# Kernel tuning notes

Measured on AMD Instinct MI355X. Metric: run time of the kernel, lower is better.

Reference implementation:

```python
import jax, jax.numpy as jnp
import numpy as np

B, T, I, H, R, O = 128, 512, 64, 512, 4, 64
NOISE_STD = 0.05
TAU = 0.2


def setup_inputs() -> dict:
    key = jax.random.key(0)
    ks = jax.random.split(key, 16)
    s = 0.08  # xavier-ish scale to keep gates in sane range
    return {
        "u": jax.random.normal(ks[0], (B, T, I), jnp.float32),
        "x0": jnp.zeros((B, H), jnp.float32),
        "noise": jax.random.normal(ks[1], (T, B, H), jnp.float32),
        "W_ir": jax.random.normal(ks[2], (H, I), jnp.float32) * s,
        "b_ir": jax.random.normal(ks[3], (H,), jnp.float32) * s,
        "W_iz": jax.random.normal(ks[4], (H, I), jnp.float32) * s,
        "b_iz": jax.random.normal(ks[5], (H,), jnp.float32) * s,
        "W_ih": jax.random.normal(ks[6], (H, I), jnp.float32) * s,
        "b_ih": jax.random.normal(ks[7], (H,), jnp.float32) * s,
        "N_hr": jax.random.normal(ks[8], (H, R), jnp.float32) * s,
        "M_hr": jax.random.normal(ks[9], (H, R), jnp.float32) * s,
        "N_hz": jax.random.normal(ks[10], (H, R), jnp.float32) * s,
        "M_hz": jax.random.normal(ks[11], (H, R), jnp.float32) * s,
        "N_hh": jax.random.normal(ks[12], (H, R), jnp.float32) * s,
        "M_hh": jax.random.normal(ks[13], (H, R), jnp.float32) * s,
        "W_out": jax.random.normal(ks[14], (O, H), jnp.float32) * s,
        "b_out": jax.random.normal(ks[15], (O,), jnp.float32) * s,
    }


def reference(u, x0, noise, W_ir, b_ir, W_iz, b_iz, W_ih, b_ih,
              N_hr, M_hr, N_hz, M_hz, N_hh, M_hh, W_out, b_out):
    scale = 1.0 / u.shape[-1] * 0 + 1.0 / N_hr.shape[0]  # 1/H (cont mode)
    scale = 1.0 / N_hr.shape[0]
    u_t = jnp.transpose(u, (1, 0, 2))  # [T,B,I]
    # precompute input projections for all steps (same math as per-step Linear)
    ir = jnp.einsum('tbi,hi->tbh', u_t, W_ir) + b_ir
    iz = jnp.einsum('tbi,hi->tbh', u_t, W_iz) + b_iz
    ih = jnp.einsum('tbi,hi->tbh', u_t, W_ih) + b_ih

    def step(x, inp):
        ir_t, iz_t, ih_t, n_t = inp
        hr = (x @ N_hr) @ M_hr.T * scale
        hz = (x @ N_hz) @ M_hz.T * scale
        r = jax.nn.sigmoid(ir_t + hr)
        z = jax.nn.sigmoid(iz_t + hz)
        hh = ((r * x) @ N_hh) @ M_hh.T * scale
        g = jnp.tanh(ih_t + hh)
        rec_x = (1.0 - z) * g + z * x
        x_new = x + NOISE_STD * n_t + TAU * (-x + rec_x)  # cont mode
        return x_new, x_new

    x_last, traj = jax.lax.scan(step, x0, (ir, iz, ih, noise))  # traj: [T,B,H]
    traj = jnp.transpose(traj, (1, 0, 2))  # [B,T,H]
    output = jnp.einsum('bth,oh->bto', traj, W_out) + b_out
    return output, x_last, traj
```

## Files before the change

kernel.cpp:

```cpp
#include <hip/hip_runtime.h>
#include <hip/hip_bf16.h>
#include <stdint.h>

#define Bv 128
#define Tv 512
#define Iv 64
#define Hv 512
#define Ov 64

typedef __attribute__((ext_vector_type(8))) short bv8;
typedef __attribute__((ext_vector_type(4))) float fv4;
typedef __attribute__((ext_vector_type(2))) float fv2;
typedef __attribute__((ext_vector_type(4))) unsigned uv4;
typedef __attribute__((ext_vector_type(2))) unsigned uv2;
typedef __attribute__((ext_vector_type(8))) unsigned short usv8;

#define LOG2E 1.44269504f
#define TWOLOG2E 2.88539008f

static __device__ __forceinline__ unsigned short f2bf(float f) {
  unsigned u = __builtin_bit_cast(unsigned, f);
  u += 0x7fffu + ((u >> 16) & 1u);
  return (unsigned short)(u >> 16);
}
static __device__ __forceinline__ float bf2f(unsigned short s) {
  return __builtin_bit_cast(float, ((unsigned)s) << 16);
}
static __device__ __forceinline__ fv2 pkfma(fv2 a, fv2 b, fv2 c) {
  return __builtin_elementwise_fma(a, b, c);
}

static __device__ __forceinline__ float wave_red(float v) {
  float d;
  asm("v_add_f32_dpp %0, %1, %1 quad_perm:[1,0,3,2] row_mask:0xf bank_mask:0xf"
      : "=v"(d) : "v"(v)); v = d;
  asm("v_add_f32_dpp %0, %1, %1 quad_perm:[2,3,0,1] row_mask:0xf bank_mask:0xf"
      : "=v"(d) : "v"(v)); v = d;
  asm("v_add_f32_dpp %0, %1, %1 row_ror:4 row_mask:0xf bank_mask:0xf"
      : "=v"(d) : "v"(v)); v = d;
  asm("v_add_f32_dpp %0, %1, %1 row_ror:8 row_mask:0xf bank_mask:0xf"
      : "=v"(d) : "v"(v)); v = d;
  unsigned a = __builtin_bit_cast(unsigned, v);
  uv2 p = __builtin_amdgcn_permlane16_swap(a, a, false, false);
  v = __builtin_bit_cast(float, p[0]) + __builtin_bit_cast(float, p[1]);
  a = __builtin_bit_cast(unsigned, v);
  uv2 q = __builtin_amdgcn_permlane32_swap(a, a, false, false);
  v = __builtin_bit_cast(float, q[0]) + __builtin_bit_cast(float, q[1]);
  return v;
}

__global__ __launch_bounds__(256) void proj_kernel(
    const float* __restrict__ u,
    const float* __restrict__ Wir, const float* __restrict__ bir,
    const float* __restrict__ Wiz, const float* __restrict__ biz,
    const float* __restrict__ Wih, const float* __restrict__ bih,
    unsigned* __restrict__ irz, unsigned short* __restrict__ ihb)
{
  __shared__ __align__(16) unsigned short As[64][72];
  const int bt0 = blockIdx.x * 64;
  const int h0b = blockIdx.y * 64;
  const int tid = threadIdx.x;
  {
    const int r = tid >> 2, ksg = (tid & 3) * 16;
    const float* src = u + (size_t)(bt0 + r) * Iv + ksg;
    unsigned short tmp[16];
#pragma unroll
    for (int i = 0; i < 16; i += 4) {
      float4 v = *(const float4*)(src + i);
      tmp[i] = f2bf(v.x); tmp[i+1] = f2bf(v.y); tmp[i+2] = f2bf(v.z); tmp[i+3] = f2bf(v.w);
    }
    *(uv4*)&As[r][ksg]     = *(uv4*)&tmp[0];
    *(uv4*)&As[r][ksg + 8] = *(uv4*)&tmp[8];
  }
  __syncthreads();
  const int wave = tid >> 6, lane = tid & 63;
  const int n = lane & 15, q = lane >> 4;
  const int h = h0b + wave * 16 + n;
  const float* Wg[3] = {Wir, Wiz, Wih};
  const float SCL[3] = {-LOG2E, -LOG2E, -TWOLOG2E};
  bv8 bfrag[3][2];
#pragma unroll
  for (int g = 0; g < 3; ++g)
#pragma unroll
    for (int ks = 0; ks < 2; ++ks) {
      const float* wp = Wg[g] + (size_t)h * Iv + ks * 32 + q * 8;
      float4 w0 = *(const float4*)wp, w1 = *(const float4*)(wp + 4);
      const float s = SCL[g];
      bv8 f;
      f[0] = (short)f2bf(w0.x * s); f[1] = (short)f2bf(w0.y * s);
      f[2] = (short)f2bf(w0.z * s); f[3] = (short)f2bf(w0.w * s);
      f[4] = (short)f2bf(w1.x * s); f[5] = (short)f2bf(w1.y * s);
      f[6] = (short)f2bf(w1.z * s); f[7] = (short)f2bf(w1.w * s);
      bfrag[g][ks] = f;
    }
  const float bs0 = bir[h] * -LOG2E, bs1 = biz[h] * -LOG2E, bs2 = bih[h] * -TWOLOG2E;
#pragma unroll
  for (int sub = 0; sub < 4; ++sub) {
    bv8 a0 = *(const bv8*)&As[sub * 16 + n][q * 8];
    bv8 a1 = *(const bv8*)&As[sub * 16 + n][32 + q * 8];
    fv4 ar = {0.f,0.f,0.f,0.f}, az = {0.f,0.f,0.f,0.f}, ah = {0.f,0.f,0.f,0.f};
    ar = __builtin_amdgcn_mfma_f32_16x16x32_bf16(a0, bfrag[0][0], ar, 0, 0, 0);
    ar = __builtin_amdgcn_mfma_f32_16x16x32_bf16(a1, bfrag[0][1], ar, 0, 0, 0);
    az = __builtin_amdgcn_mfma_f32_16x16x32_bf16(a0, bfrag[1][0], az, 0, 0, 0);
    az = __builtin_amdgcn_mfma_f32_16x16x32_bf16(a1, bfrag[1][1], az, 0, 0, 0);
    ah = __builtin_amdgcn_mfma_f32_16x16x32_bf16(a0, bfrag[2][0], ah, 0, 0, 0);
    ah = __builtin_amdgcn_mfma_f32_16x16x32_bf16(a1, bfrag[2][1], ah, 0, 0, 0);
#pragma unroll
    for (int j = 0; j < 4; ++j) {
      const int row = bt0 + sub * 16 + q * 4 + j;
      const size_t slot = (size_t)row * Hv + h;
      irz[slot] = ((unsigned)f2bf(az[j] + bs1) << 16) | (unsigned)f2bf(ar[j] + bs0);
      ihb[slot] = f2bf(ah[j] + bs2);
    }
  }
}

struct Buf { uv4 irz0, irz1; usv8 ih; fv4 nz0, nz1; };
#define IRZ(bf, j) ((j) < 4 ? (bf).irz0[(j)] : (bf).irz1[(j) - 4])
#define NZE(bf, j) ((j) < 4 ? (bf).nz0[(j)]  : (bf).nz1[(j) - 4])

__global__ __launch_bounds__(64, 1) void scan_kernel(
    const float* __restrict__ x0, const float* __restrict__ noise,
    const float* __restrict__ Nhr, const float* __restrict__ Mhr,
    const float* __restrict__ Nhz, const float* __restrict__ Mhz,
    const float* __restrict__ Nhh, const float* __restrict__ Mhh,
    unsigned* __restrict__ traj, const unsigned short* __restrict__ ihb,
    float* __restrict__ xlast)
{
  __shared__ __align__(16) float S[7 * 2048];
  const int b = blockIdx.x, lane = threadIdx.x;
  const int h0 = lane * 8;
  const int xr = (lane & 7) * 4;

  int fo[8];
#pragma unroll
  for (int j = 0; j < 8; ++j) fo[j] = lane * 32 + ((j * 4) ^ xr);

#define LDQ(sec, j) (*(const fv4*)&S[(sec) * 2048 + fo[j]])

  {
    const float smr = -(1.0f / 512.0f) * LOG2E;
    const float smh = -(1.0f / 512.0f) * TWOLOG2E;
#pragma unroll
    for (int j = 0; j < 8; ++j) {
      *(fv4*)&S[0 * 2048 + fo[j]] = *(const fv4*)(Nhr + (size_t)(h0 + j) * 4);
      *(fv4*)&S[1 * 2048 + fo[j]] = *(const fv4*)(Nhz + (size_t)(h0 + j) * 4);
      *(fv4*)&S[2 * 2048 + fo[j]] = *(const fv4*)(Nhh + (size_t)(h0 + j) * 4);
      fv4 mr = *(const fv4*)(Mhr + (size_t)(h0 + j) * 4) * smr;
      fv4 mz = *(const fv4*)(Mhz + (size_t)(h0 + j) * 4) * smr;
      fv4 q0 = {mr[0], mz[0], mr[1], mz[1]};
      fv4 q1 = {mr[2], mz[2], mr[3], mz[3]};
      *(fv4*)&S[3 * 2048 + fo[j]] = q0;
      *(fv4*)&S[4 * 2048 + fo[j]] = q1;
    }
#pragma unroll
    for (int p = 0; p < 4; ++p) {
      fv4 a = *(const fv4*)(Mhh + (size_t)(h0 + 2 * p) * 4) * smh;
      fv4 c = *(const fv4*)(Mhh + (size_t)(h0 + 2 * p + 1) * 4) * smh;
      fv4 q0 = {a[0], c[0], a[1], c[1]};
      fv4 q1 = {a[2], c[2], a[3], c[3]};
      *(fv4*)&S[5 * 2048 + fo[p]] = q0;
      *(fv4*)&S[6 * 2048 + fo[p]] = q1;
    }
  }

  float x[8];
  {
    const float* xp = x0 + (size_t)b * Hv;
    fv4 a = *(const fv4*)(xp + h0);
    fv4 c = *(const fv4*)(xp + h0 + 4);
#pragma unroll
    for (int j = 0; j < 4; ++j) { x[j] = a[j]; x[j + 4] = c[j]; }
  }
  const unsigned* trajU = traj + (size_t)b * Tv * Hv;
  const unsigned short* ihU = ihb + (size_t)b * Tv * Hv;
  const float* noiseU = noise + (size_t)b * Hv;

  Buf A, Bb;
  auto LOAD = [&](Buf& bf, int t) {
    const unsigned* pr = trajU + (size_t)t * Hv;
    bf.irz0 = *(const uv4*)(pr + h0);
    bf.irz1 = *(const uv4*)(pr + h0 + 4);
    const unsigned short* pi = ihU + (size_t)t * Hv;
    bf.ih = *(const usv8*)(pi + h0);
    const float* pn = noiseU + (size_t)t * (Bv * Hv);
    bf.nz0 = *(const fv4*)(pn + h0);
    bf.nz1 = *(const fv4*)(pn + h0 + 4);
  };
  auto PIN = [&](Buf& bf) {
    asm volatile("" : "+v"(bf.irz0), "+v"(bf.irz1), "+v"(bf.ih),
                      "+v"(bf.nz0), "+v"(bf.nz1));
  };
  auto STEP = [&](const Buf& bf, int t) {
    fv2 sr01 = {0.f,0.f}, sr23 = {0.f,0.f}, sz01 = {0.f,0.f}, sz23 = {0.f,0.f};
#pragma unroll
    for (int j = 0; j < 8; ++j) {
      fv4 nrj = LDQ(0, j), nzj = LDQ(1, j);
      fv2 xs = {x[j], x[j]};
      sr01 = pkfma(xs, fv2{nrj[0], nrj[1]}, sr01);
      sr23 = pkfma(xs, fv2{nrj[2], nrj[3]}, sr23);
      sz01 = pkfma(xs, fv2{nzj[0], nzj[1]}, sz01);
      sz23 = pkfma(xs, fv2{nzj[2], nzj[3]}, sz23);
    }
    float sr[4] = {sr01[0], sr01[1], sr23[0], sr23[1]};
    float sz[4] = {sz01[0], sz01[1], sz23[0], sz23[1]};
#pragma unroll
    for (int r = 0; r < 4; ++r) { sr[r] = wave_red(sr[r]); sz[r] = wave_red(sz[r]); }
    fv2 srz[4];
#pragma unroll
    for (int r = 0; r < 4; ++r) srz[r] = fv2{sr[r], sz[r]};
    float rxv[8], w02[8];
#pragma unroll
    for (int j = 0; j < 8; ++j) {
      fv4 q0 = LDQ(3, j), q1 = LDQ(4, j);
      fv2 h2 = fv2{q1[2], q1[3]} * srz[3];
      h2 = pkfma(fv2{q1[0], q1[1]}, srz[2], h2);
      h2 = pkfma(fv2{q0[2], q0[3]}, srz[1], h2);
      h2 = pkfma(fv2{q0[0], q0[1]}, srz[0], h2);
      unsigned w = IRZ(bf, j);
      float tr = h2[0] + __builtin_bit_cast(float, w << 16);
      float tz = h2[1] + __builtin_bit_cast(float, w & 0xffff0000u);
      float er = __builtin_amdgcn_exp2f(tr);
      float ez = __builtin_amdgcn_exp2f(tz);
      float Ar = 1.0f + er, Az = 1.0f + ez;
      float R = __builtin_amdgcn_rcpf(Ar * Az);
      rxv[j] = (R * Az) * x[j];
      w02[j] = fmaf(R * Ar, -0.2f, 0.2f);
    }
    fv2 sh01 = {0.f,0.f}, sh23 = {0.f,0.f};
#pragma unroll
    for (int j = 0; j < 8; ++j) {
      fv4 nhj = LDQ(2, j);
      fv2 xs = {rxv[j], rxv[j]};
      sh01 = pkfma(xs, fv2{nhj[0], nhj[1]}, sh01);
      sh23 = pkfma(xs, fv2{nhj[2], nhj[3]}, sh23);
    }
    fv2 sh2[4];
    {
      float s0 = wave_red(sh01[0]), s1 = wave_red(sh01[1]);
      float s2 = wave_red(sh23[0]), s3 = wave_red(sh23[1]);
      sh2[0] = fv2{s0, s0}; sh2[1] = fv2{s1, s1};
      sh2[2] = fv2{s2, s2}; sh2[3] = fv2{s3, s3};
    }
#pragma unroll
    for (int p = 0; p < 4; ++p) {
      fv4 q0 = LDQ(5, p), q1 = LDQ(6, p);
      fv2 hh = fv2{q1[2], q1[3]} * sh2[3];
      hh = pkfma(fv2{q1[0], q1[1]}, sh2[2], hh);
      hh = pkfma(fv2{q0[2], q0[3]}, sh2[1], hh);
      hh = pkfma(fv2{q0[0], q0[1]}, sh2[0], hh);
      const int j0 = 2 * p, j1 = 2 * p + 1;
      float t0 = fminf(hh[0] + bf2f(bf.ih[j0]), 44.0f);
      float t1 = fminf(hh[1] + bf2f(bf.ih[j1]), 44.0f);
      float e0 = __builtin_amdgcn_exp2f(t0);
      float e1 = __builtin_amdgcn_exp2f(t1);
      float A0 = 1.0f + e0, A1 = 1.0f + e1;
      float R = __builtin_amdgcn_rcpf(A0 * A1);
      float g0 = (1.0f - e0) * A1 * R;
      float g1 = (1.0f - e1) * A0 * R;
      float d0 = g0 - x[j0], d1 = g1 - x[j1];
      x[j0] = fmaf(0.05f, NZE(bf, j0), x[j0]);
      x[j0] = fmaf(w02[j0], d0, x[j0]);
      x[j1] = fmaf(0.05f, NZE(bf, j1), x[j1]);
      x[j1] = fmaf(w02[j1], d1, x[j1]);
    }
    float* po = (float*)(trajU + (size_t)t * Hv);
    fv4 s0 = {x[0], x[1], x[2], x[3]}, s1 = {x[4], x[5], x[6], x[7]};
    *(fv4*)(po + h0) = s0;
    *(fv4*)(po + h0 + 4) = s1;
  };
  LOAD(A, 0);
  for (int t = 0; t < Tv; t += 2) {
    LOAD(Bb, t + 1);
    STEP(A, t);
    PIN(Bb);
    if (t + 2 < Tv) LOAD(A, t + 2);
    STEP(Bb, t + 1);
    PIN(A);
  }
  {
    float* xp = xlast + (size_t)b * Hv;
    fv4 s0 = {x[0], x[1], x[2], x[3]}, s1 = {x[4], x[5], x[6], x[7]};
    *(fv4*)(xp + h0) = s0;
    *(fv4*)(xp + h0 + 4) = s1;
  }
#undef LDQ
}

__global__ __launch_bounds__(256) void outproj_kernel(
    const float* __restrict__ traj, const float* __restrict__ Wout,
    const float* __restrict__ bout, float* __restrict__ out)
{
  __shared__ __align__(16) unsigned short As[64][40];
  const int bt0 = blockIdx.x * 64;
  const int tid = threadIdx.x;
  const int wave = tid >> 6, lane = tid & 63;
  const int n = lane & 15, q = lane >> 4;
  const int o = wave * 16 + n;
  const float bo = bout[o];
  fv4 acc[4] = {{0.f,0.f,0.f,0.f},{0.f,0.f,0.f,0.f},{0.f,0.f,0.f,0.f},{0.f,0.f,0.f,0.f}};
  const int r = tid >> 2, ksg = (tid & 3) * 8;
  for (int ks = 0; ks < 16; ++ks) {
    __syncthreads();
    {
      const float* src = traj + (size_t)(bt0 + r) * Hv + ks * 32 + ksg;
      float4 v0 = *(const float4*)src, v1 = *(const float4*)(src + 4);
      unsigned short tmp[8];
      tmp[0] = f2bf(v0.x); tmp[1] = f2bf(v0.y); tmp[2] = f2bf(v0.z); tmp[3] = f2bf(v0.w);
      tmp[4] = f2bf(v1.x); tmp[5] = f2bf(v1.y); tmp[6] = f2bf(v1.z); tmp[7] = f2bf(v1.w);
      *(uv4*)&As[r][ksg] = *(uv4*)&tmp[0];
    }
    __syncthreads();
    const float* wp = Wout + (size_t)o * Hv + ks * 32 + q * 8;
    float4 w0 = *(const float4*)wp, w1 = *(const float4*)(wp + 4);
    bv8 bf;
    bf[0] = (short)f2bf(w0.x); bf[1] = (short)f2bf(w0.y);
    bf[2] = (short)f2bf(w0.z); bf[3] = (short)f2bf(w0.w);
    bf[4] = (short)f2bf(w1.x); bf[5] = (short)f2bf(w1.y);
    bf[6] = (short)f2bf(w1.z); bf[7] = (short)f2bf(w1.w);
#pragma unroll
    for (int sub = 0; sub < 4; ++sub) {
      bv8 af = *(const bv8*)&As[sub * 16 + n][q * 8];
      acc[sub] = __builtin_amdgcn_mfma_f32_16x16x32_bf16(af, bf, acc[sub], 0, 0, 0);
    }
  }
#pragma unroll
  for (int sub = 0; sub < 4; ++sub)
#pragma unroll
    for (int j = 0; j < 4; ++j) {
      const int row = bt0 + sub * 16 + q * 4 + j;
      out[(size_t)row * Ov + o] = acc[sub][j] + bo;
    }
}

extern "C" void kernel_launch(void* const* d_in, const int* in_sizes, int n_in,
                              void* d_out, int out_size, void* d_ws, size_t ws_size,
                              hipStream_t stream) {
  const float* u    = (const float*)d_in[0];
  const float* x0   = (const float*)d_in[1];
  const float* noise= (const float*)d_in[2];
  const float* Wir  = (const float*)d_in[3];
  const float* bir  = (const float*)d_in[4];
  const float* Wiz  = (const float*)d_in[5];
  const float* biz  = (const float*)d_in[6];
  const float* Wih  = (const float*)d_in[7];
  const float* bih  = (const float*)d_in[8];
  const float* Nhr  = (const float*)d_in[9];
  const float* Mhr  = (const float*)d_in[10];
  const float* Nhz  = (const float*)d_in[11];
  const float* Mhz  = (const float*)d_in[12];
  const float* Nhh  = (const float*)d_in[13];
  const float* Mhh  = (const float*)d_in[14];
  const float* Wout = (const float*)d_in[15];
  const float* bout = (const float*)d_in[16];

  float* out   = (float*)d_out;
  float* xlast = out + (size_t)Bv * Tv * Ov;
  float* traj  = xlast + (size_t)Bv * Hv;
  unsigned short* ihbuf = (unsigned short*)d_ws;

  proj_kernel<<<dim3(1024, 8, 1), 256, 0, stream>>>(
      u, Wir, bir, Wiz, biz, Wih, bih, (unsigned*)traj, ihbuf);
  scan_kernel<<<dim3(128, 1, 1), 64, 0, stream>>>(
      x0, noise, Nhr, Mhr, Nhz, Mhz, Nhh, Mhh, (unsigned*)traj, ihbuf, xlast);
  outproj_kernel<<<dim3(1024, 1, 1), 256, 0, stream>>>(traj, Wout, bout, out);
}
```

Baseline: 833.8 us.

## Stream per-step scan inputs into LDS via global_load_lds double buffering

The scan kernel's per-step prefetch of gate pre-activations, the ih projection and noise used to go through registers in a two-buffer scheme. It now uses direct global-to-LDS 16-byte DMA loads into two LDS stream buffers, issued two steps ahead. An explicit vmcnt wait gates the reads, and the data is read back from LDS just before use. This is meant to free VGPRs and hide global latency on the serial recurrence, at the cost of extra LDS round trips and a hand-tuned waitcnt count that depends on stores also counting in vmcnt. The Mhh coefficient table is also packed into one LDS section.

```diff
diff --git a/kernel.cpp b/kernel.cpp
--- a/kernel.cpp
+++ b/kernel.cpp
@@ -28,6 +28,12 @@
 }
 static __device__ __forceinline__ fv2 pkfma(fv2 a, fv2 b, fv2 c) {
   return __builtin_elementwise_fma(a, b, c);
+}
+
+static __device__ __forceinline__ void dma16(const void* g, void* l) {
+  __builtin_amdgcn_global_load_lds(
+      (const __attribute__((address_space(1))) void*)g,
+      (__attribute__((address_space(3))) void*)l, 16, 0, 0);
 }
 
 static __device__ __forceinline__ float wave_red(float v) {
@@ -115,9 +121,14 @@
   }
 }
 
-struct Buf { uv4 irz0, irz1; usv8 ih; fv4 nz0, nz1; };
-#define IRZ(bf, j) ((j) < 4 ? (bf).irz0[(j)] : (bf).irz1[(j) - 4])
-#define NZE(bf, j) ((j) < 4 ? (bf).nz0[(j)]  : (bf).nz1[(j) - 4])
+#define OFF_NR 0
+#define OFF_NZ 2048
+#define OFF_NH 4096
+#define OFF_MRZ0 6144
+#define OFF_MRZ1 8192
+#define OFF_MH2 10240
+#define STREAM0 49152
+#define STREAM_SZ 5120
 
 __global__ __launch_bounds__(64, 1) void scan_kernel(
     const float* __restrict__ x0, const float* __restrict__ noise,
@@ -127,31 +138,33 @@
     unsigned* __restrict__ traj, const unsigned short* __restrict__ ihb,
     float* __restrict__ xlast)
 {
-  __shared__ __align__(16) float S[7 * 2048];
+  __shared__ __align__(16) float S[12288 + 2560];
   const int b = blockIdx.x, lane = threadIdx.x;
   const int h0 = lane * 8;
   const int xr = (lane & 7) * 4;
+  const int lofs16 = lane * 16;
+  const int lofs32 = lane * 32;
 
   int fo[8];
 #pragma unroll
   for (int j = 0; j < 8; ++j) fo[j] = lane * 32 + ((j * 4) ^ xr);
 
-#define LDQ(sec, j) (*(const fv4*)&S[(sec) * 2048 + fo[j]])
+#define LDQ(sec, j) (*(const fv4*)&S[(sec) + fo[j]])
 
   {
     const float smr = -(1.0f / 512.0f) * LOG2E;
     const float smh = -(1.0f / 512.0f) * TWOLOG2E;
 #pragma unroll
     for (int j = 0; j < 8; ++j) {
-      *(fv4*)&S[0 * 2048 + fo[j]] = *(const fv4*)(Nhr + (size_t)(h0 + j) * 4);
-      *(fv4*)&S[1 * 2048 + fo[j]] = *(const fv4*)(Nhz + (size_t)(h0 + j) * 4);
-      *(fv4*)&S[2 * 2048 + fo[j]] = *(const fv4*)(Nhh + (size_t)(h0 + j) * 4);
+      *(fv4*)&S[OFF_NR + fo[j]] = *(const fv4*)(Nhr + (size_t)(h0 + j) * 4);
+      *(fv4*)&S[OFF_NZ + fo[j]] = *(const fv4*)(Nhz + (size_t)(h0 + j) * 4);
+      *(fv4*)&S[OFF_NH + fo[j]] = *(const fv4*)(Nhh + (size_t)(h0 + j) * 4);
       fv4 mr = *(const fv4*)(Mhr + (size_t)(h0 + j) * 4) * smr;
       fv4 mz = *(const fv4*)(Mhz + (size_t)(h0 + j) * 4) * smr;
       fv4 q0 = {mr[0], mz[0], mr[1], mz[1]};
       fv4 q1 = {mr[2], mz[2], mr[3], mz[3]};
-      *(fv4*)&S[3 * 2048 + fo[j]] = q0;
-      *(fv4*)&S[4 * 2048 + fo[j]] = q1;
+      *(fv4*)&S[OFF_MRZ0 + fo[j]] = q0;
+      *(fv4*)&S[OFF_MRZ1 + fo[j]] = q1;
     }
 #pragma unroll
     for (int p = 0; p < 4; ++p) {
@@ -159,8 +172,8 @@
       fv4 c = *(const fv4*)(Mhh + (size_t)(h0 + 2 * p + 1) * 4) * smh;
       fv4 q0 = {a[0], c[0], a[1], c[1]};
       fv4 q1 = {a[2], c[2], a[3], c[3]};
-      *(fv4*)&S[5 * 2048 + fo[p]] = q0;
-      *(fv4*)&S[6 * 2048 + fo[p]] = q1;
+      *(fv4*)&S[OFF_MH2 + fo[p]]     = q0;
+      *(fv4*)&S[OFF_MH2 + fo[p + 4]] = q1;
     }
   }
 
@@ -175,27 +188,24 @@
   const unsigned* trajU = traj + (size_t)b * Tv * Hv;
   const unsigned short* ihU = ihb + (size_t)b * Tv * Hv;
   const float* noiseU = noise + (size_t)b * Hv;
-
-  Buf A, Bb;
-  auto LOAD = [&](Buf& bf, int t) {
-    const unsigned* pr = trajU + (size_t)t * Hv;
-    bf.irz0 = *(const uv4*)(pr + h0);
-    bf.irz1 = *(const uv4*)(pr + h0 + 4);
-    const unsigned short* pi = ihU + (size_t)t * Hv;
-    bf.ih = *(const usv8*)(pi + h0);
-    const float* pn = noiseU + (size_t)t * (Bv * Hv);
-    bf.nz0 = *(const fv4*)(pn + h0);
-    bf.nz1 = *(const fv4*)(pn + h0 + 4);
+  char* Sb = (char*)S;
+
+  auto ISSUE = [&](int sb, int t) {
+    const char* g1 = (const char*)(trajU + (size_t)t * Hv) + lofs16;
+    dma16(g1,        Sb + sb);
+    dma16(g1 + 1024, Sb + sb + 1024);
+    const char* g2 = (const char*)(ihU + (size_t)t * Hv) + lofs16;
+    dma16(g2,        Sb + sb + 2048);
+    const char* g3 = (const char*)(noiseU + (size_t)t * (Bv * Hv)) + lofs16;
+    dma16(g3,        Sb + sb + 3072);
+    dma16(g3 + 1024, Sb + sb + 3072 + 1024);
   };
-  auto PIN = [&](Buf& bf) {
-    asm volatile("" : "+v"(bf.irz0), "+v"(bf.irz1), "+v"(bf.ih),
-                      "+v"(bf.nz0), "+v"(bf.nz1));
-  };
-  auto STEP = [&](const Buf& bf, int t) {
+
+  auto STEP = [&](int sb, int t) {
     fv2 sr01 = {0.f,0.f}, sr23 = {0.f,0.f}, sz01 = {0.f,0.f}, sz23 = {0.f,0.f};
 #pragma unroll
     for (int j = 0; j < 8; ++j) {
-      fv4 nrj = LDQ(0, j), nzj = LDQ(1, j);
+      fv4 nrj = LDQ(OFF_NR, j), nzj = LDQ(OFF_NZ, j);
       fv2 xs = {x[j], x[j]};
       sr01 = pkfma(xs, fv2{nrj[0], nrj[1]}, sr01);
       sr23 = pkfma(xs, fv2{nrj[2], nrj[3]}, sr23);
@@ -209,15 +219,19 @@
     fv2 srz[4];
 #pragma unroll
     for (int r = 0; r < 4; ++r) srz[r] = fv2{sr[r], sz[r]};
+    asm volatile("s_waitcnt vmcnt(5)" ::: "memory");
+    __builtin_amdgcn_sched_barrier(0);
+    uv4 irz0 = *(const uv4*)(Sb + sb + lofs32);
+    uv4 irz1 = *(const uv4*)(Sb + sb + lofs32 + 16);
     float rxv[8], w02[8];
 #pragma unroll
     for (int j = 0; j < 8; ++j) {
-      fv4 q0 = LDQ(3, j), q1 = LDQ(4, j);
+      fv4 q0 = LDQ(OFF_MRZ0, j), q1 = LDQ(OFF_MRZ1, j);
       fv2 h2 = fv2{q1[2], q1[3]} * srz[3];
       h2 = pkfma(fv2{q1[0], q1[1]}, srz[2], h2);
       h2 = pkfma(fv2{q0[2], q0[3]}, srz[1], h2);
       h2 = pkfma(fv2{q0[0], q0[1]}, srz[0], h2);
-      unsigned w = IRZ(bf, j);
+      unsigned w = (j < 4) ? irz0[j] : irz1[j - 4];
       float tr = h2[0] + __builtin_bit_cast(float, w << 16);
       float tz = h2[1] + __builtin_bit_cast(float, w & 0xffff0000u);
       float er = __builtin_amdgcn_exp2f(tr);
@@ -230,7 +244,7 @@
     fv2 sh01 = {0.f,0.f}, sh23 = {0.f,0.f};
 #pragma unroll
     for (int j = 0; j < 8; ++j) {
-      fv4 nhj = LDQ(2, j);
+      fv4 nhj = LDQ(OFF_NH, j);
       fv2 xs = {rxv[j], rxv[j]};
       sh01 = pkfma(xs, fv2{nhj[0], nhj[1]}, sh01);
       sh23 = pkfma(xs, fv2{nhj[2], nhj[3]}, sh23);
@@ -242,16 +256,20 @@
       sh2[0] = fv2{s0, s0}; sh2[1] = fv2{s1, s1};
       sh2[2] = fv2{s2, s2}; sh2[3] = fv2{s3, s3};
     }
+    usv8 ihv = *(const usv8*)(Sb + sb + 2048 + lofs16);
+    fv4 nz0 = *(const fv4*)(Sb + sb + 3072 + lofs32);
+    fv4 nz1 = *(const fv4*)(Sb + sb + 3072 + lofs32 + 16);
 #pragma unroll
     for (int p = 0; p < 4; ++p) {
-      fv4 q0 = LDQ(5, p), q1 = LDQ(6, p);
+      fv4 q0 = *(const fv4*)&S[OFF_MH2 + fo[p]];
+      fv4 q1 = *(const fv4*)&S[OFF_MH2 + fo[p + 4]];
       fv2 hh = fv2{q1[2], q1[3]} * sh2[3];
       hh = pkfma(fv2{q1[0], q1[1]}, sh2[2], hh);
       hh = pkfma(fv2{q0[2], q0[3]}, sh2[1], hh);
       hh = pkfma(fv2{q0[0], q0[1]}, sh2[0], hh);
       const int j0 = 2 * p, j1 = 2 * p + 1;
-      float t0 = fminf(hh[0] + bf2f(bf.ih[j0]), 44.0f);
-      float t1 = fminf(hh[1] + bf2f(bf.ih[j1]), 44.0f);
+      float t0 = fminf(hh[0] + bf2f(ihv[j0]), 44.0f);
+      float t1 = fminf(hh[1] + bf2f(ihv[j1]), 44.0f);
       float e0 = __builtin_amdgcn_exp2f(t0);
       float e1 = __builtin_amdgcn_exp2f(t1);
       float A0 = 1.0f + e0, A1 = 1.0f + e1;
@@ -259,24 +277,26 @@
       float g0 = (1.0f - e0) * A1 * R;
       float g1 = (1.0f - e1) * A0 * R;
       float d0 = g0 - x[j0], d1 = g1 - x[j1];
-      x[j0] = fmaf(0.05f, NZE(bf, j0), x[j0]);
+      float n0 = (j0 < 4) ? nz0[j0] : nz1[j0 - 4];
+      float n1 = (j1 < 4) ? nz0[j1] : nz1[j1 - 4];
+      x[j0] = fmaf(0.05f, n0, x[j0]);
       x[j0] = fmaf(w02[j0], d0, x[j0]);
-      x[j1] = fmaf(0.05f, NZE(bf, j1), x[j1]);
+      x[j1] = fmaf(0.05f, n1, x[j1]);
       x[j1] = fmaf(w02[j1], d1, x[j1]);
     }
     float* po = (float*)(trajU + (size_t)t * Hv);
     fv4 s0 = {x[0], x[1], x[2], x[3]}, s1 = {x[4], x[5], x[6], x[7]};
     *(fv4*)(po + h0) = s0;
     *(fv4*)(po + h0 + 4) = s1;
+    int tn = t + 2 > Tv - 1 ? Tv - 1 : t + 2;
+    ISSUE(sb, tn);
   };
-  LOAD(A, 0);
+
+  ISSUE(STREAM0, 0);
+  ISSUE(STREAM0 + STREAM_SZ, 1);
   for (int t = 0; t < Tv; t += 2) {
-    LOAD(Bb, t + 1);
-    STEP(A, t);
-    PIN(Bb);
-    if (t + 2 < Tv) LOAD(A, t + 2);
-    STEP(Bb, t + 1);
-    PIN(A);
+    STEP(STREAM0, t);
+    STEP(STREAM0 + STREAM_SZ, t + 1);
   }
   {
     float* xp = xlast + (size_t)b * Hv;
```

New measurement: 823.0 us. About the same (-1.3%).
